# Performance work log

Measured on AMD Instinct MI355X. Metric: run time of the kernel, lower is better.

Reference implementation:

```python
import jax, jax.numpy as jnp
import numpy as np

N_NODES = 100000
N_EDGES = 1600000
D_IN, D_HID, D_OUT = 128, 128, 64


def setup_inputs() -> dict:
    key = jax.random.key(0)
    ks = jax.random.split(key, 8)
    x = jax.random.normal(ks[0], (N_NODES, D_IN), dtype=jnp.float32)
    edge_index = jax.random.randint(ks[1], (2, N_EDGES), 0, N_NODES, dtype=jnp.int64)
    def glorot(k, fan_in, fan_out):
        s = jnp.sqrt(6.0 / (fan_in + fan_out))
        return jax.random.uniform(k, (fan_in, fan_out), jnp.float32, -s, s)
    return {
        "x": x,
        "edge_index": edge_index,
        "W1": glorot(ks[2], D_IN, D_HID), "b1": jnp.zeros((D_HID,), jnp.float32),
        "W2": glorot(ks[3], D_HID, D_HID), "b2": jnp.zeros((D_HID,), jnp.float32),
        "W3": glorot(ks[4], D_HID, D_OUT), "b3": jnp.zeros((D_OUT,), jnp.float32),
    }


def _gcn_norm(edge_index, n_nodes):
    # add self-loops, compute symmetric normalization D^-1/2 A D^-1/2
    loop = jnp.arange(n_nodes, dtype=edge_index.dtype)
    src = jnp.concatenate([edge_index[0], loop])  # message source
    dst = jnp.concatenate([edge_index[1], loop])  # aggregation target
    deg = jax.ops.segment_sum(jnp.ones_like(dst, dtype=jnp.float32), dst,
                              num_segments=n_nodes)
    dinv = jnp.where(deg > 0, jax.lax.rsqrt(deg), 0.0)
    norm = dinv[src] * dinv[dst]  # [E + N]
    return src, dst, norm


def _gcn_conv(x, W, b, src, dst, norm, n_nodes):
    xw = x @ W                                # dense transform [N, F_out]
    msg = xw[src] * norm[:, None]             # gather + scale   [E+N, F_out]
    out = jax.ops.segment_sum(msg, dst, num_segments=n_nodes)  # scatter-add
    return out + b


def reference(x, edge_index, W1, b1, W2, b2, W3, b3):
    n = x.shape[0]
    src, dst, norm = _gcn_norm(edge_index, n)  # cached=True: same norm reused
    h = jax.nn.relu(_gcn_conv(x, W1, b1, src, dst, norm, n))
    h = jax.nn.relu(_gcn_conv(h, W2, b2, src, dst, norm, n))
    return _gcn_conv(h, W3, b3, src, dst, norm, n)
```

## Files before the change

### kernel.cpp

```cpp
#include <hip/hip_runtime.h>
#include <hip/hip_fp16.h>


#define NN 100000
#define NE 1600000
#define TT (NE + NN)
#define BSH 9
#define NBUCK ((NN + 511) / 512)
#define EPB1 16384
#define NPB1 ((TT + EPB1 - 1) / EPB1)

typedef _Float16 f16x8 __attribute__((ext_vector_type(8)));
typedef float f32x4 __attribute__((ext_vector_type(4)));


__global__ __launch_bounds__(256) void bucket_count(const int* __restrict__ ei,
                                                    int* __restrict__ gbc) {
    __shared__ int hist[NBUCK];
    const int tid = threadIdx.x;
    const int base = blockIdx.x * EPB1;
    for (int b = tid; b < NBUCK; b += 256) hist[b] = 0;
    __syncthreads();
    for (int i = tid; i < EPB1; i += 256) {
        int e = base + i;
        if (e >= TT) break;
        int d = (e < NE) ? ei[NE + e] : (e - NE);
        atomicAdd(&hist[d >> BSH], 1);
    }
    __syncthreads();
    for (int b = tid; b < NBUCK; b += 256)
        if (hist[b]) atomicAdd(&gbc[b], hist[b]);
}


__global__ __launch_bounds__(256) void scan_buckets(const int* __restrict__ gbc,
                                                    int* __restrict__ bbase,
                                                    int* __restrict__ gcursor,
                                                    int* __restrict__ rowptr) {
    __shared__ int s[256];
    const int t = threadIdx.x;
    int v = (t < NBUCK) ? gbc[t] : 0;
    s[t] = v;
    __syncthreads();
    for (int off = 1; off < 256; off <<= 1) {
        int u = (t >= off) ? s[t - off] : 0;
        __syncthreads();
        s[t] += u;
        __syncthreads();
    }
    if (t < NBUCK) {
        int excl = s[t] - v;
        bbase[t] = excl;
        gcursor[t] = excl;
    }
    if (t == 0) { bbase[NBUCK] = TT; rowptr[NN] = TT; }
}


__global__ __launch_bounds__(256) void partition_p1(const int* __restrict__ ei,
                                                    int* __restrict__ gcursor,
                                                    int* __restrict__ part) {
    __shared__ int hist[NBUCK];
    const int tid = threadIdx.x;
    const int base = blockIdx.x * EPB1;
    for (int b = tid; b < NBUCK; b += 256) hist[b] = 0;
    __syncthreads();
    for (int i = tid; i < EPB1; i += 256) {
        int e = base + i;
        if (e >= TT) break;
        int d = (e < NE) ? ei[NE + e] : (e - NE);
        atomicAdd(&hist[d >> BSH], 1);
    }
    __syncthreads();
    for (int b = tid; b < NBUCK; b += 256) {
        int cnt = hist[b];
        hist[b] = cnt ? atomicAdd(&gcursor[b], cnt) : 0;
    }
    __syncthreads();
    for (int i = tid; i < EPB1; i += 256) {
        int e = base + i;
        if (e >= TT) break;
        int s, d;
        if (e < NE) { s = ei[e]; d = ei[NE + e]; }
        else        { s = d = e - NE; }
        int pos = atomicAdd(&hist[d >> BSH], 1);
        part[pos] = s | ((d & 511) << 17);
    }
}


__global__ __launch_bounds__(256) void partition_p2(const int* __restrict__ part,
                                                    const int* __restrict__ bbase,
                                                    int* __restrict__ rowptr,
                                                    float* __restrict__ dinv,
                                                    int* __restrict__ col) {
    __shared__ int cnt[512];
    __shared__ int scn[512];
    __shared__ int cur[512];
    const int b = blockIdx.x;
    const int v0 = b << BSH;
    const int nv = min(512, NN - v0);
    const int tid = threadIdx.x;
    const int base = bbase[b];
    const int nrec = bbase[b + 1] - base;

    cnt[tid] = 0; cnt[tid + 256] = 0;
    __syncthreads();
    for (int i = tid; i < nrec; i += 256)
        atomicAdd(&cnt[((unsigned)part[base + i]) >> 17], 1);
    __syncthreads();
    scn[tid] = cnt[tid]; scn[tid + 256] = cnt[tid + 256];
    __syncthreads();
    for (int off = 1; off < 512; off <<= 1) {
        int a = (tid >= off) ? scn[tid - off] : 0;
        int c = (tid + 256 >= off) ? scn[tid + 256 - off] : 0;
        __syncthreads();
        scn[tid] += a; scn[tid + 256] += c;
        __syncthreads();
    }
#pragma unroll
    for (int p = 0; p < 2; p++) {
        int j = tid + p * 256;
        if (j < nv) {
            int excl = scn[j] - cnt[j];
            rowptr[v0 + j] = base + excl;
            dinv[v0 + j] = rsqrtf((float)cnt[j]);
            cur[j] = base + excl;
        }
    }
    __syncthreads();
    for (int i = tid; i < nrec; i += 256) {
        int r = part[base + i];
        int pos = atomicAdd(&cur[((unsigned)r) >> 17], 1);
        col[pos] = r & 0x1FFFF;
    }
}


__global__ __launch_bounds__(256) void wt_conv_all(const float* __restrict__ W1,
                                                   const float* __restrict__ W2,
                                                   const float* __restrict__ W3,
                                                   _Float16* __restrict__ Wt1,
                                                   _Float16* __restrict__ Wt2,
                                                   _Float16* __restrict__ Wt3) {
    int idx = blockIdx.x * 256 + threadIdx.x;
    if (idx < 16384) {
        Wt1[(idx % 128) * 128 + idx / 128] = (_Float16)W1[idx];
    } else if (idx < 32768) {
        int i = idx - 16384;
        Wt2[(i % 128) * 128 + i / 128] = (_Float16)W2[i];
    } else if (idx < 40960) {
        int i = idx - 32768;
        Wt3[(i % 64) * 128 + i / 64] = (_Float16)W3[i];
    }
}


template <int F, bool AHALF>
__global__ __launch_bounds__(256) void gemm_mfma(const void* __restrict__ Ap,
                                                 const _Float16* __restrict__ Wt,
                                                 const float* __restrict__ dinv,
                                                 __half* __restrict__ Yh) {
    constexpr int NT = F / 16;
    __shared__ _Float16 Yl[64][136];

    const int tid = threadIdx.x;
    const int wave = tid >> 6;
    const int lane = tid & 63;
    const int m = lane & 15;
    const int q = lane >> 4;
    const int grow0 = blockIdx.x * 64;
    const int row = grow0 + wave * 16 + m;
    const bool rok = row < NN;

    f32x4 acc[NT];
#pragma unroll
    for (int t = 0; t < NT; t++) acc[t] = (f32x4){0.f, 0.f, 0.f, 0.f};

#pragma unroll
    for (int kt = 0; kt < 128; kt += 32) {
        const int k0 = kt + q * 8;
        union { f16x8 v; _Float16 e[8]; } au;
        if (rok) {
            if constexpr (AHALF) {
                au.v = *reinterpret_cast<const f16x8*>(
                    (const __half*)Ap + (size_t)row * 128 + k0);
            } else {
                const float* A = (const float*)Ap;
                float4 x0 = *reinterpret_cast<const float4*>(A + (size_t)row * 128 + k0);
                float4 x1 = *reinterpret_cast<const float4*>(A + (size_t)row * 128 + k0 + 4);
                au.e[0] = (_Float16)x0.x; au.e[1] = (_Float16)x0.y;
                au.e[2] = (_Float16)x0.z; au.e[3] = (_Float16)x0.w;
                au.e[4] = (_Float16)x1.x; au.e[5] = (_Float16)x1.y;
                au.e[6] = (_Float16)x1.z; au.e[7] = (_Float16)x1.w;
            }
        } else {
#pragma unroll
            for (int j = 0; j < 8; j++) au.e[j] = (_Float16)0.f;
        }
#pragma unroll
        for (int t = 0; t < NT; t++) {
            f16x8 bf = *reinterpret_cast<const f16x8*>(Wt + (t * 16 + m) * 128 + k0);
            acc[t] = __builtin_amdgcn_mfma_f32_16x16x32_f16(au.v, bf, acc[t], 0, 0, 0);
        }
    }
#pragma unroll
    for (int r = 0; r < 4; r++) {
        int lrow = wave * 16 + q * 4 + r;
        int gr = grow0 + lrow;
        float s = (gr < NN) ? dinv[gr] : 0.f;
#pragma unroll
        for (int t = 0; t < NT; t++)
            Yl[lrow][t * 16 + m] = (_Float16)(s * acc[t][r]);
    }
    __syncthreads();
    constexpr int CH = F / 8;
    for (int i = tid; i < 64 * CH; i += 256) {
        int lrow = i / CH, c = i % CH;
        int gr = grow0 + lrow;
        if (gr < NN)
            *reinterpret_cast<f16x8*>(Yh + (size_t)gr * F + c * 8) =
                *reinterpret_cast<const f16x8*>(&Yl[lrow][c * 8]);
    }
}


__device__ __forceinline__ void acc_add8(float* acc, float4 raw) {
    const __half2* h2 = reinterpret_cast<const __half2*>(&raw);
#pragma unroll
    for (int qq = 0; qq < 4; qq++) {
        float2 fv = __half22float2(h2[qq]);
        acc[2 * qq]     += fv.x;
        acc[2 * qq + 1] += fv.y;
    }
}


template <int FOUT>
__global__ __launch_bounds__(256) void fused_agg_gemm(
        const __half* __restrict__ XWh,
        const int* __restrict__ rowptr,
        const int* __restrict__ col,
        const float* __restrict__ dinv,
        const float* __restrict__ bias,
        const _Float16* __restrict__ Wt,
        __half* __restrict__ Yout) {
    __shared__ _Float16 Hs[16][136];
    __shared__ _Float16 Ds[16][FOUT + 8];

    const int tid = threadIdx.x;
    const int v0 = blockIdx.x * 16;

    {
        const int lnode = tid >> 4;
        const int f = tid & 15;
        const int v = v0 + lnode;
        const int beg = rowptr[v];
        const int end = rowptr[v + 1];
        const float4* base = reinterpret_cast<const float4*>(XWh);
        float acc[8] = {0.f, 0.f, 0.f, 0.f, 0.f, 0.f, 0.f, 0.f};
#pragma unroll 4
        for (int e = beg; e < end; e++) {
            int u = col[e];
            float4 raw = base[(size_t)u * 16 + f];
            acc_add8(acc, raw);
        }
        const float dv = dinv[v];
        union { f16x8 v8; _Float16 e8[8]; } hu;
#pragma unroll
        for (int qq = 0; qq < 8; qq++) {
            float r = dv * acc[qq] + bias[f * 8 + qq];
            hu.e8[qq] = (_Float16)fmaxf(r, 0.f);
        }
        *reinterpret_cast<f16x8*>(&Hs[lnode][f * 8]) = hu.v8;
    }
    __syncthreads();

    constexpr int TPW = FOUT / 64;
    const int wave = tid >> 6;
    const int lane = tid & 63;
    const int m = lane & 15;
    const int q = lane >> 4;
    f32x4 gacc[TPW];
#pragma unroll
    for (int t = 0; t < TPW; t++) gacc[t] = (f32x4){0.f, 0.f, 0.f, 0.f};
#pragma unroll
    for (int kt = 0; kt < 128; kt += 32) {
        const int k0 = kt + q * 8;
        f16x8 av = *reinterpret_cast<const f16x8*>(&Hs[m][k0]);
#pragma unroll
        for (int t = 0; t < TPW; t++) {
            const int gc = (wave * TPW + t) * 16 + m;
            f16x8 bv = *reinterpret_cast<const f16x8*>(Wt + gc * 128 + k0);
            gacc[t] = __builtin_amdgcn_mfma_f32_16x16x32_f16(av, bv, gacc[t], 0, 0, 0);
        }
    }
#pragma unroll
    for (int r = 0; r < 4; r++) {
        const int lrow = q * 4 + r;
        const float s = dinv[v0 + lrow];
#pragma unroll
        for (int t = 0; t < TPW; t++)
            Ds[lrow][(wave * TPW + t) * 16 + m] = (_Float16)(s * gacc[t][r]);
    }
    __syncthreads();
    constexpr int CH = FOUT / 8;
    for (int i2 = tid; i2 < 16 * CH; i2 += 256) {
        int lrow = i2 / CH, c = i2 % CH;
        *reinterpret_cast<f16x8*>(Yout + (size_t)(v0 + lrow) * FOUT + c * 8) =
            *reinterpret_cast<const f16x8*>(&Ds[lrow][c * 8]);
    }
}


__global__ __launch_bounds__(256) void agg_final(
        const __half* __restrict__ XWh,
        const int* __restrict__ rowptr,
        const int* __restrict__ col,
        const float* __restrict__ dinv,
        const float* __restrict__ bias,
        float* __restrict__ out) {
    constexpr int TPN = 8;
    constexpr int NPB = 256 / TPN;
    const int v = blockIdx.x * NPB + threadIdx.x / TPN;
    const int f = threadIdx.x % TPN;
    const int beg = rowptr[v];
    const int end = rowptr[v + 1];
    const float4* base = reinterpret_cast<const float4*>(XWh);
    float acc[8] = {0.f, 0.f, 0.f, 0.f, 0.f, 0.f, 0.f, 0.f};
#pragma unroll 4
    for (int e = beg; e < end; e++) {
        int u = col[e];
        float4 raw = base[(size_t)u * TPN + f];
        acc_add8(acc, raw);
    }
    const float dv = dinv[v];
    float r[8];
#pragma unroll
    for (int q = 0; q < 8; q++)
        r[q] = dv * acc[q] + bias[f * 8 + q];
    float* op = out + (size_t)v * 64 + f * 8;
    *reinterpret_cast<float4*>(op)     = make_float4(r[0], r[1], r[2], r[3]);
    *reinterpret_cast<float4*>(op + 4) = make_float4(r[4], r[5], r[6], r[7]);
}


extern "C" void kernel_launch(void* const* d_in, const int* in_sizes, int n_in,
                              void* d_out, int out_size, void* d_ws, size_t ws_size,
                              hipStream_t stream) {
    const float* x  = (const float*)d_in[0];
    const int*   ei = (const int*)d_in[1];
    const float* W1 = (const float*)d_in[2];
    const float* b1 = (const float*)d_in[3];
    const float* W2 = (const float*)d_in[4];
    const float* b2 = (const float*)d_in[5];
    const float* W3 = (const float*)d_in[6];
    const float* b3 = (const float*)d_in[7];
    float* out = (float*)d_out;

    char* p = (char*)d_ws;
    int*      rowptr  = (int*)p;       p += 400016;
    float*    dinv    = (float*)p;     p += 400000;
    int*      gbc     = (int*)p;       p += 1024;
    int*      bbase   = (int*)p;       p += 1024;
    int*      gcursor = (int*)p;       p += 1024;
    _Float16* Wt1     = (_Float16*)p;  p += 32768;
    _Float16* Wt2     = (_Float16*)p;  p += 32768;
    _Float16* Wt3     = (_Float16*)p;  p += 16384;
    int*      part    = (int*)p;       p += (size_t)TT * 4;
    int*      col     = (int*)p;       p += (size_t)TT * 4;
    __half*   xwh1    = (__half*)p;    p += (size_t)NN * 128 * 2;
    __half*   xwh2    = (__half*)p;
    __half*   xwh3    = xwh1;

    hipMemsetAsync(gbc, 0, NBUCK * 4, stream);
    wt_conv_all<<<160, 256, 0, stream>>>(W1, W2, W3, Wt1, Wt2, Wt3);
    bucket_count<<<NPB1, 256, 0, stream>>>(ei, gbc);
    scan_buckets<<<1, 256, 0, stream>>>(gbc, bbase, gcursor, rowptr);
    partition_p1<<<NPB1, 256, 0, stream>>>(ei, gcursor, part);
    partition_p2<<<NBUCK, 256, 0, stream>>>(part, bbase, rowptr, dinv, col);

    const int gb = (NN + 63) / 64;
    const int fb = NN / 16;
    gemm_mfma<128, false><<<gb, 256, 0, stream>>>(x, Wt1, dinv, xwh1);
    fused_agg_gemm<128><<<fb, 256, 0, stream>>>(xwh1, rowptr, col, dinv, b1,
                                                Wt2, xwh2);
    fused_agg_gemm<64><<<fb, 256, 0, stream>>>(xwh2, rowptr, col, dinv, b2,
                                               Wt3, xwh3);
    agg_final<<<NN / 32, 256, 0, stream>>>(xwh3, rowptr, col, dinv, b3, out);
}
```

Baseline: 455.8 us.

## Sort nodes by degree within buckets to balance aggregation work per block

Adds a per-bucket counting sort of nodes by in-degree (capped at 63) that builds a permutation array, and has the aggregation kernels process nodes in that permuted order. Nodes of similar degree then share a block or wavefront, which is meant to cut divergence and idle lanes in the edge loops. The cost is an extra perm read per node, less contiguous node access and scattered output rows, plus extra work in partition_p2.

```diff
diff --git a/kernel.cpp b/kernel.cpp
--- a/kernel.cpp
+++ b/kernel.cpp
@@ -93,10 +93,12 @@
                                                     const int* __restrict__ bbase,
                                                     int* __restrict__ rowptr,
                                                     float* __restrict__ dinv,
-                                                    int* __restrict__ col) {
+                                                    int* __restrict__ col,
+                                                    int* __restrict__ perm) {
     __shared__ int cnt[512];
     __shared__ int scn[512];
     __shared__ int cur[512];
+    __shared__ int dbs[64];
     const int b = blockIdx.x;
     const int v0 = b << BSH;
     const int nv = min(512, NN - v0);
@@ -133,6 +135,28 @@
         int r = part[base + i];
         int pos = atomicAdd(&cur[((unsigned)r) >> 17], 1);
         col[pos] = r & 0x1FFFF;
+    }
+    if (tid < 64) dbs[tid] = 0;
+    __syncthreads();
+#pragma unroll
+    for (int p = 0; p < 2; p++) {
+        int j = tid + p * 256;
+        if (j < nv) atomicAdd(&dbs[min(cnt[j], 63)], 1);
+    }
+    __syncthreads();
+    if (tid == 0) {
+        int s = 0;
+#pragma unroll
+        for (int i = 0; i < 64; i++) { int c = dbs[i]; dbs[i] = s; s += c; }
+    }
+    __syncthreads();
+#pragma unroll
+    for (int p = 0; p < 2; p++) {
+        int j = tid + p * 256;
+        if (j < nv) {
+            int pos = atomicAdd(&dbs[min(cnt[j], 63)], 1);
+            perm[v0 + pos] = v0 + j;
+        }
     }
 }
 
@@ -244,17 +268,21 @@
         const float* __restrict__ dinv,
         const float* __restrict__ bias,
         const _Float16* __restrict__ Wt,
+        const int* __restrict__ perm,
         __half* __restrict__ Yout) {
     __shared__ _Float16 Hs[16][136];
     __shared__ _Float16 Ds[16][FOUT + 8];
+    __shared__ int pvs[16];
 
     const int tid = threadIdx.x;
     const int v0 = blockIdx.x * 16;
+    if (tid < 16) pvs[tid] = perm[v0 + tid];
+    __syncthreads();
 
     {
         const int lnode = tid >> 4;
         const int f = tid & 15;
-        const int v = v0 + lnode;
+        const int v = pvs[lnode];
         const int beg = rowptr[v];
         const int end = rowptr[v + 1];
         const float4* base = reinterpret_cast<const float4*>(XWh);
@@ -298,7 +326,7 @@
 #pragma unroll
     for (int r = 0; r < 4; r++) {
         const int lrow = q * 4 + r;
-        const float s = dinv[v0 + lrow];
+        const float s = dinv[pvs[lrow]];
 #pragma unroll
         for (int t = 0; t < TPW; t++)
             Ds[lrow][(wave * TPW + t) * 16 + m] = (_Float16)(s * gacc[t][r]);
@@ -307,7 +335,7 @@
     constexpr int CH = FOUT / 8;
     for (int i2 = tid; i2 < 16 * CH; i2 += 256) {
         int lrow = i2 / CH, c = i2 % CH;
-        *reinterpret_cast<f16x8*>(Yout + (size_t)(v0 + lrow) * FOUT + c * 8) =
+        *reinterpret_cast<f16x8*>(Yout + (size_t)pvs[lrow] * FOUT + c * 8) =
             *reinterpret_cast<const f16x8*>(&Ds[lrow][c * 8]);
     }
 }
@@ -319,10 +347,11 @@
         const int* __restrict__ col,
         const float* __restrict__ dinv,
         const float* __restrict__ bias,
+        const int* __restrict__ perm,
         float* __restrict__ out) {
     constexpr int TPN = 8;
     constexpr int NPB = 256 / TPN;
-    const int v = blockIdx.x * NPB + threadIdx.x / TPN;
+    const int v = perm[blockIdx.x * NPB + threadIdx.x / TPN];
     const int f = threadIdx.x % TPN;
     const int beg = rowptr[v];
     const int end = rowptr[v + 1];
@@ -361,6 +390,7 @@
     char* p = (char*)d_ws;
     int*      rowptr  = (int*)p;       p += 400016;
     float*    dinv    = (float*)p;     p += 400000;
+    int*      perm    = (int*)p;       p += 400000;
     int*      gbc     = (int*)p;       p += 1024;
     int*      bbase   = (int*)p;       p += 1024;
     int*      gcursor = (int*)p;       p += 1024;
@@ -378,14 +408,14 @@
     bucket_count<<<NPB1, 256, 0, stream>>>(ei, gbc);
     scan_buckets<<<1, 256, 0, stream>>>(gbc, bbase, gcursor, rowptr);
     partition_p1<<<NPB1, 256, 0, stream>>>(ei, gcursor, part);
-    partition_p2<<<NBUCK, 256, 0, stream>>>(part, bbase, rowptr, dinv, col);
+    partition_p2<<<NBUCK, 256, 0, stream>>>(part, bbase, rowptr, dinv, col, perm);
 
     const int gb = (NN + 63) / 64;
     const int fb = NN / 16;
     gemm_mfma<128, false><<<gb, 256, 0, stream>>>(x, Wt1, dinv, xwh1);
     fused_agg_gemm<128><<<fb, 256, 0, stream>>>(xwh1, rowptr, col, dinv, b1,
-                                                Wt2, xwh2);
+                                                Wt2, perm, xwh2);
     fused_agg_gemm<64><<<fb, 256, 0, stream>>>(xwh2, rowptr, col, dinv, b2,
-                                               Wt3, xwh3);
-    agg_final<<<NN / 32, 256, 0, stream>>>(xwh3, rowptr, col, dinv, b3, out);
-}
+                                               Wt3, perm, xwh3);
+    agg_final<<<NN / 32, 256, 0, stream>>>(xwh3, rowptr, col, dinv, b3, perm, out);
+}
```

Result: slower. 496.2 us (+8.9%).

## Make each wave own four nodes end-to-end, replacing block barriers with wave barriers

Applied to the files above, without the earlier changes.

In the fused aggregation+GEMM kernel, each wave now aggregates its own 4 nodes and runs the full-width MFMA transform on those rows alone. The result is written out by that same wave, so the two block-wide __syncthreads become wave barriers. The aim is to stop fast waves stalling on the slowest node's neighbour loop when node degrees vary. In exchange each wave issues all FOUT/16 MFMA tiles, with 16-row tiles carrying only 4 distinct rows. It also loads the full weight matrix from global memory, which is four times the MFMA and weight-load work per wave.

```diff
diff --git a/kernel.cpp b/kernel.cpp
--- a/kernel.cpp
+++ b/kernel.cpp
@@ -249,12 +249,15 @@
     __shared__ _Float16 Ds[16][FOUT + 8];
 
     const int tid = threadIdx.x;
+    const int wave = tid >> 6;
+    const int lane = tid & 63;
+    const int w4 = wave * 4;
     const int v0 = blockIdx.x * 16;
 
     {
-        const int lnode = tid >> 4;
-        const int f = tid & 15;
-        const int v = v0 + lnode;
+        const int lnode = lane >> 4;
+        const int f = lane & 15;
+        const int v = v0 + w4 + lnode;
         const int beg = rowptr[v];
         const int end = rowptr[v + 1];
         const float4* base = reinterpret_cast<const float4*>(XWh);
@@ -272,41 +275,36 @@
             float r = dv * acc[qq] + bias[f * 8 + qq];
             hu.e8[qq] = (_Float16)fmaxf(r, 0.f);
         }
-        *reinterpret_cast<f16x8*>(&Hs[lnode][f * 8]) = hu.v8;
-    }
-    __syncthreads();
-
-    constexpr int TPW = FOUT / 64;
-    const int wave = tid >> 6;
-    const int lane = tid & 63;
+        *reinterpret_cast<f16x8*>(&Hs[w4 + lnode][f * 8]) = hu.v8;
+    }
+    __builtin_amdgcn_wave_barrier();
+
+    constexpr int NT = FOUT / 16;
     const int m = lane & 15;
     const int q = lane >> 4;
-    f32x4 gacc[TPW];
-#pragma unroll
-    for (int t = 0; t < TPW; t++) gacc[t] = (f32x4){0.f, 0.f, 0.f, 0.f};
+    f32x4 gacc[NT];
+#pragma unroll
+    for (int t = 0; t < NT; t++) gacc[t] = (f32x4){0.f, 0.f, 0.f, 0.f};
 #pragma unroll
     for (int kt = 0; kt < 128; kt += 32) {
         const int k0 = kt + q * 8;
-        f16x8 av = *reinterpret_cast<const f16x8*>(&Hs[m][k0]);
-#pragma unroll
-        for (int t = 0; t < TPW; t++) {
-            const int gc = (wave * TPW + t) * 16 + m;
-            f16x8 bv = *reinterpret_cast<const f16x8*>(Wt + gc * 128 + k0);
+        f16x8 av = *reinterpret_cast<const f16x8*>(&Hs[w4 + (m & 3)][k0]);
+#pragma unroll
+        for (int t = 0; t < NT; t++) {
+            f16x8 bv = *reinterpret_cast<const f16x8*>(Wt + (t * 16 + m) * 128 + k0);
             gacc[t] = __builtin_amdgcn_mfma_f32_16x16x32_f16(av, bv, gacc[t], 0, 0, 0);
         }
     }
-#pragma unroll
-    for (int r = 0; r < 4; r++) {
-        const int lrow = q * 4 + r;
-        const float s = dinv[v0 + lrow];
-#pragma unroll
-        for (int t = 0; t < TPW; t++)
-            Ds[lrow][(wave * TPW + t) * 16 + m] = (_Float16)(s * gacc[t][r]);
-    }
-    __syncthreads();
+    {
+        const float s = dinv[v0 + w4 + q];
+#pragma unroll
+        for (int t = 0; t < NT; t++)
+            Ds[w4 + q][t * 16 + m] = (_Float16)(s * gacc[t][q]);
+    }
+    __builtin_amdgcn_wave_barrier();
     constexpr int CH = FOUT / 8;
-    for (int i2 = tid; i2 < 16 * CH; i2 += 256) {
-        int lrow = i2 / CH, c = i2 % CH;
+    for (int i2 = lane; i2 < 4 * CH; i2 += 64) {
+        int lrow = w4 + i2 / CH, c = i2 % CH;
         *reinterpret_cast<f16x8*>(Yout + (size_t)(v0 + lrow) * FOUT + c * 8) =
             *reinterpret_cast<const f16x8*>(&Ds[lrow][c * 8]);
     }
```

Result: slower. 520.7 us (+14.3%).

## Fuse graph preprocessing kernels into one cooperative kernel with grid syncs

Applied to the files above, without the earlier changes.

Replaces the memset, weight-transpose and the four CSR-building kernels (bucket count, scan, two partition passes) with a single cooperative kernel of NBUCK blocks. The stages are separated by grid.sync, and the counter zeroing moves into the first stage. The aim is to remove several kernel launches and the gaps between them. In exchange it adds four grid-wide barriers. Most blocks sit idle in the single-block scan stage, and the 104-block partition stages leave the rest of the grid idle.

```diff
diff --git a/kernel.cpp b/kernel.cpp
--- a/kernel.cpp
+++ b/kernel.cpp
@@ -1,5 +1,8 @@
 #include <hip/hip_runtime.h>
 #include <hip/hip_fp16.h>
+#include <hip/hip_cooperative_groups.h>
+
+namespace cg = cooperative_groups;
 
 
 #define NN 100000
@@ -14,144 +17,138 @@
 typedef float f32x4 __attribute__((ext_vector_type(4)));
 
 
-__global__ __launch_bounds__(256) void bucket_count(const int* __restrict__ ei,
-                                                    int* __restrict__ gbc) {
+__global__ __launch_bounds__(256) void prep_all(
+        const int* __restrict__ ei,
+        const float* __restrict__ W1, const float* __restrict__ W2,
+        const float* __restrict__ W3,
+        _Float16* __restrict__ Wt1, _Float16* __restrict__ Wt2,
+        _Float16* __restrict__ Wt3,
+        int* __restrict__ gbc, int* __restrict__ bbase,
+        int* __restrict__ gcursor,
+        int* __restrict__ rowptr, float* __restrict__ dinv,
+        int* __restrict__ part, int* __restrict__ col) {
+    cg::grid_group grid = cg::this_grid();
     __shared__ int hist[NBUCK];
+    __shared__ int sA[512];
+    __shared__ int sB[512];
+    __shared__ int sC[512];
     const int tid = threadIdx.x;
-    const int base = blockIdx.x * EPB1;
-    for (int b = tid; b < NBUCK; b += 256) hist[b] = 0;
-    __syncthreads();
-    for (int i = tid; i < EPB1; i += 256) {
-        int e = base + i;
-        if (e >= TT) break;
-        int d = (e < NE) ? ei[NE + e] : (e - NE);
-        atomicAdd(&hist[d >> BSH], 1);
-    }
-    __syncthreads();
-    for (int b = tid; b < NBUCK; b += 256)
-        if (hist[b]) atomicAdd(&gbc[b], hist[b]);
-}
-
-
-__global__ __launch_bounds__(256) void scan_buckets(const int* __restrict__ gbc,
-                                                    int* __restrict__ bbase,
-                                                    int* __restrict__ gcursor,
-                                                    int* __restrict__ rowptr) {
-    __shared__ int s[256];
-    const int t = threadIdx.x;
-    int v = (t < NBUCK) ? gbc[t] : 0;
-    s[t] = v;
-    __syncthreads();
-    for (int off = 1; off < 256; off <<= 1) {
-        int u = (t >= off) ? s[t - off] : 0;
-        __syncthreads();
-        s[t] += u;
-        __syncthreads();
-    }
-    if (t < NBUCK) {
-        int excl = s[t] - v;
-        bbase[t] = excl;
-        gcursor[t] = excl;
-    }
-    if (t == 0) { bbase[NBUCK] = TT; rowptr[NN] = TT; }
-}
-
-
-__global__ __launch_bounds__(256) void partition_p1(const int* __restrict__ ei,
-                                                    int* __restrict__ gcursor,
-                                                    int* __restrict__ part) {
-    __shared__ int hist[NBUCK];
-    const int tid = threadIdx.x;
-    const int base = blockIdx.x * EPB1;
-    for (int b = tid; b < NBUCK; b += 256) hist[b] = 0;
-    __syncthreads();
-    for (int i = tid; i < EPB1; i += 256) {
-        int e = base + i;
-        if (e >= TT) break;
-        int d = (e < NE) ? ei[NE + e] : (e - NE);
-        atomicAdd(&hist[d >> BSH], 1);
-    }
-    __syncthreads();
-    for (int b = tid; b < NBUCK; b += 256) {
-        int cnt = hist[b];
-        hist[b] = cnt ? atomicAdd(&gcursor[b], cnt) : 0;
-    }
-    __syncthreads();
-    for (int i = tid; i < EPB1; i += 256) {
-        int e = base + i;
-        if (e >= TT) break;
-        int s, d;
-        if (e < NE) { s = ei[e]; d = ei[NE + e]; }
-        else        { s = d = e - NE; }
-        int pos = atomicAdd(&hist[d >> BSH], 1);
-        part[pos] = s | ((d & 511) << 17);
-    }
-}
-
-
-__global__ __launch_bounds__(256) void partition_p2(const int* __restrict__ part,
-                                                    const int* __restrict__ bbase,
-                                                    int* __restrict__ rowptr,
-                                                    float* __restrict__ dinv,
-                                                    int* __restrict__ col) {
-    __shared__ int cnt[512];
-    __shared__ int scn[512];
-    __shared__ int cur[512];
     const int b = blockIdx.x;
-    const int v0 = b << BSH;
-    const int nv = min(512, NN - v0);
-    const int tid = threadIdx.x;
-    const int base = bbase[b];
-    const int nrec = bbase[b + 1] - base;
-
-    cnt[tid] = 0; cnt[tid + 256] = 0;
-    __syncthreads();
-    for (int i = tid; i < nrec; i += 256)
-        atomicAdd(&cnt[((unsigned)part[base + i]) >> 17], 1);
-    __syncthreads();
-    scn[tid] = cnt[tid]; scn[tid + 256] = cnt[tid + 256];
-    __syncthreads();
-    for (int off = 1; off < 512; off <<= 1) {
-        int a = (tid >= off) ? scn[tid - off] : 0;
-        int c = (tid + 256 >= off) ? scn[tid + 256 - off] : 0;
-        __syncthreads();
-        scn[tid] += a; scn[tid + 256] += c;
-        __syncthreads();
-    }
-#pragma unroll
-    for (int p = 0; p < 2; p++) {
-        int j = tid + p * 256;
-        if (j < nv) {
-            int excl = scn[j] - cnt[j];
-            rowptr[v0 + j] = base + excl;
-            dinv[v0 + j] = rsqrtf((float)cnt[j]);
-            cur[j] = base + excl;
-        }
-    }
-    __syncthreads();
-    for (int i = tid; i < nrec; i += 256) {
-        int r = part[base + i];
-        int pos = atomicAdd(&cur[((unsigned)r) >> 17], 1);
-        col[pos] = r & 0x1FFFF;
-    }
-}
-
-
-__global__ __launch_bounds__(256) void wt_conv_all(const float* __restrict__ W1,
-                                                   const float* __restrict__ W2,
-                                                   const float* __restrict__ W3,
-                                                   _Float16* __restrict__ Wt1,
-                                                   _Float16* __restrict__ Wt2,
-                                                   _Float16* __restrict__ Wt3) {
-    int idx = blockIdx.x * 256 + threadIdx.x;
-    if (idx < 16384) {
-        Wt1[(idx % 128) * 128 + idx / 128] = (_Float16)W1[idx];
-    } else if (idx < 32768) {
-        int i = idx - 16384;
-        Wt2[(i % 128) * 128 + i / 128] = (_Float16)W2[i];
-    } else if (idx < 40960) {
-        int i = idx - 32768;
-        Wt3[(i % 64) * 128 + i / 64] = (_Float16)W3[i];
+
+    {
+        int idx = b * 256 + tid;
+        if (idx < 16384) {
+            Wt1[(idx % 128) * 128 + idx / 128] = (_Float16)W1[idx];
+        } else if (idx < 32768) {
+            int i = idx - 16384;
+            Wt2[(i % 128) * 128 + i / 128] = (_Float16)W2[i];
+        } else if (idx < 40960) {
+            int i = idx - 32768;
+            Wt3[(i % 64) * 128 + i / 64] = (_Float16)W3[i];
+        }
+        if (idx < NBUCK) gbc[idx] = 0;
+        if (idx == 0) { bbase[NBUCK] = TT; rowptr[NN] = TT; }
+    }
+    grid.sync();
+
+    if (b < NPB1) {
+        for (int i = tid; i < NBUCK; i += 256) hist[i] = 0;
+        __syncthreads();
+        const int base = b * EPB1;
+        for (int i = tid; i < EPB1; i += 256) {
+            int e = base + i;
+            if (e >= TT) break;
+            int d = (e < NE) ? ei[NE + e] : (e - NE);
+            atomicAdd(&hist[d >> BSH], 1);
+        }
+        __syncthreads();
+        for (int i = tid; i < NBUCK; i += 256)
+            if (hist[i]) atomicAdd(&gbc[i], hist[i]);
+    }
+    grid.sync();
+
+    if (b == 0) {
+        int v = (tid < NBUCK) ? gbc[tid] : 0;
+        sA[tid] = v;
+        __syncthreads();
+        for (int off = 1; off < 256; off <<= 1) {
+            int u = (tid >= off) ? sA[tid - off] : 0;
+            __syncthreads();
+            sA[tid] += u;
+            __syncthreads();
+        }
+        if (tid < NBUCK) {
+            int excl = sA[tid] - v;
+            bbase[tid] = excl;
+            gcursor[tid] = excl;
+        }
+    }
+    grid.sync();
+
+    if (b < NPB1) {
+        for (int i = tid; i < NBUCK; i += 256) hist[i] = 0;
+        __syncthreads();
+        const int base = b * EPB1;
+        for (int i = tid; i < EPB1; i += 256) {
+            int e = base + i;
+            if (e >= TT) break;
+            int d = (e < NE) ? ei[NE + e] : (e - NE);
+            atomicAdd(&hist[d >> BSH], 1);
+        }
+        __syncthreads();
+        for (int i = tid; i < NBUCK; i += 256) {
+            int cnt = hist[i];
+            hist[i] = cnt ? atomicAdd(&gcursor[i], cnt) : 0;
+        }
+        __syncthreads();
+        for (int i = tid; i < EPB1; i += 256) {
+            int e = base + i;
+            if (e >= TT) break;
+            int s, d;
+            if (e < NE) { s = ei[e]; d = ei[NE + e]; }
+            else        { s = d = e - NE; }
+            int pos = atomicAdd(&hist[d >> BSH], 1);
+            part[pos] = s | ((d & 511) << 17);
+        }
+    }
+    grid.sync();
+
+    {
+        const int v0 = b << BSH;
+        const int nv = min(512, NN - v0);
+        const int base = bbase[b];
+        const int nrec = bbase[b + 1] - base;
+
+        sA[tid] = 0; sA[tid + 256] = 0;
+        __syncthreads();
+        for (int i = tid; i < nrec; i += 256)
+            atomicAdd(&sA[((unsigned)part[base + i]) >> 17], 1);
+        __syncthreads();
+        sB[tid] = sA[tid]; sB[tid + 256] = sA[tid + 256];
+        __syncthreads();
+        for (int off = 1; off < 512; off <<= 1) {
+            int a = (tid >= off) ? sB[tid - off] : 0;
+            int c = (tid + 256 >= off) ? sB[tid + 256 - off] : 0;
+            __syncthreads();
+            sB[tid] += a; sB[tid + 256] += c;
+            __syncthreads();
+        }
+#pragma unroll
+        for (int p = 0; p < 2; p++) {
+            int j = tid + p * 256;
+            if (j < nv) {
+                int excl = sB[j] - sA[j];
+                rowptr[v0 + j] = base + excl;
+                dinv[v0 + j] = rsqrtf((float)sA[j]);
+                sC[j] = base + excl;
+            }
+        }
+        __syncthreads();
+        for (int i = tid; i < nrec; i += 256) {
+            int r = part[base + i];
+            int pos = atomicAdd(&sC[((unsigned)r) >> 17], 1);
+            col[pos] = r & 0x1FFFF;
+        }
     }
 }
 
@@ -348,8 +345,8 @@
 extern "C" void kernel_launch(void* const* d_in, const int* in_sizes, int n_in,
                               void* d_out, int out_size, void* d_ws, size_t ws_size,
                               hipStream_t stream) {
+    const int*   ei = (const int*)d_in[1];
     const float* x  = (const float*)d_in[0];
-    const int*   ei = (const int*)d_in[1];
     const float* W1 = (const float*)d_in[2];
     const float* b1 = (const float*)d_in[3];
     const float* W2 = (const float*)d_in[4];
@@ -373,12 +370,15 @@
     __half*   xwh2    = (__half*)p;
     __half*   xwh3    = xwh1;
 
-    hipMemsetAsync(gbc, 0, NBUCK * 4, stream);
-    wt_conv_all<<<160, 256, 0, stream>>>(W1, W2, W3, Wt1, Wt2, Wt3);
-    bucket_count<<<NPB1, 256, 0, stream>>>(ei, gbc);
-    scan_buckets<<<1, 256, 0, stream>>>(gbc, bbase, gcursor, rowptr);
-    partition_p1<<<NPB1, 256, 0, stream>>>(ei, gcursor, part);
-    partition_p2<<<NBUCK, 256, 0, stream>>>(part, bbase, rowptr, dinv, col);
+    {
+        void* pargs[] = {(void*)&ei, (void*)&W1, (void*)&W2, (void*)&W3,
+                         (void*)&Wt1, (void*)&Wt2, (void*)&Wt3,
+                         (void*)&gbc, (void*)&bbase, (void*)&gcursor,
+                         (void*)&rowptr, (void*)&dinv,
+                         (void*)&part, (void*)&col};
+        hipLaunchCooperativeKernel((void*)prep_all, dim3(NBUCK), dim3(256),
+                                   pargs, 0, stream);
+    }
 
     const int gb = (NN + 63) / 64;
     const int fb = NN / 16;
```

After: 549.2 us. 20.5% more time.
